# Optimization experiments

Hardware: AMD Instinct MI355X
Metric: run time of the kernel (lower is better)

## Reference

```python
import jax, jax.numpy as jnp
import numpy as np

FRAME, PROJ, MID, HID, T, B = 2048, 512, 128, 1024, 48, 512


def _uniform(key, shape, stdv):
    return jax.random.uniform(key, shape, jnp.float32, -stdv, stdv)


def setup_inputs() -> dict:
    key = jax.random.key(0)
    ks = jax.random.split(key, 16)
    sp = 1.0 / np.sqrt(FRAME)   # frame_embed init
    s1 = 1.0 / np.sqrt(HID)     # LSTMCell init (1/sqrt(hidden))
    sbd = 1.0 / np.sqrt(PROJ)   # BoundaryDetector init (1/sqrt(i_features))
    return {
        "video_feats": jax.random.normal(ks[0], (B, T, FRAME), jnp.float32),
        # frame_embed: Linear(frame_size, projected_size)
        "We": _uniform(ks[1], (PROJ, FRAME), sp),
        "be": _uniform(ks[2], (PROJ,), sp),
        # lstm1: LSTMCell(projected, hidden) with bias
        "W1_ih": _uniform(ks[3], (4 * HID, PROJ), s1),
        "W1_hh": _uniform(ks[4], (4 * HID, HID), s1),
        "b1_ih": _uniform(ks[5], (4 * HID,), s1),
        "b1_hh": _uniform(ks[6], (4 * HID,), s1),
        # lstm2: LSTMCell(hidden, hidden), bias=False
        "W2_ih": _uniform(ks[7], (4 * HID, HID), s1),
        "W2_hh": _uniform(ks[8], (4 * HID, HID), s1),
        # BoundaryDetector params
        "Wsi": _uniform(ks[9], (MID, PROJ), sbd),
        "Wsh": _uniform(ks[10], (MID, HID), sbd),
        "bbd": _uniform(ks[11], (MID,), sbd),
        "vs": _uniform(ks[12], (1, MID), sbd),
    }


def _lstm_cell(x, h, c, W_ih, W_hh, b):
    gates = x @ W_ih.T + h @ W_hh.T + b  # [B, 4H]
    i, f, g, o = jnp.split(gates, 4, axis=-1)  # PyTorch gate order i,f,g,o
    i, f, o = jax.nn.sigmoid(i), jax.nn.sigmoid(f), jax.nn.sigmoid(o)
    g = jnp.tanh(g)
    c_new = f * c + i * g
    h_new = o * jnp.tanh(c_new)
    return h_new, c_new


def _binary_gate(z):
    # eval mode: threshold 0.5; straight-through identity backward
    hard = (z > 0.5).astype(z.dtype)
    return z + jax.lax.stop_gradient(hard - z)


def reference(video_feats, We, be, W1_ih, W1_hh, b1_ih, b1_hh, W2_ih, W2_hh, Wsi, Wsh, bbd, vs):
    bsz = video_feats.shape[0]
    # frame embedding (dropout is identity in eval mode)
    v = video_feats @ We.T + be  # [B, T, PROJ]
    v_t = jnp.swapaxes(v, 0, 1)  # [T, B, PROJ]
    b1 = b1_ih + b1_hh
    zeros = jnp.zeros((bsz, HID), video_feats.dtype)

    def step(carry, vt):
        h1, c1, h2, c2 = carry
        z = jax.nn.sigmoid((vt @ Wsi.T + h1 @ Wsh.T + bbd) @ vs.T)  # [B, 1]
        s = _binary_gate(z)
        h1n, c1n = _lstm_cell(vt, h1, c1, W1_ih, W1_hh, b1)
        h2n, c2n = _lstm_cell(h1n * s, h2, c2, W2_ih, W2_hh, 0.0)
        h1n = h1n * (1.0 - s)
        c1n = c1n * (1.0 - s)
        return (h1n, c1n, h2n, c2n), None

    (h1, _, _, _), _ = jax.lax.scan(step, (zeros, zeros, zeros, zeros), v_t)
    return h1
```

## Files before the change

### kernel.cpp

```cpp
#include <hip/hip_runtime.h>

#define B_     512
#define T_     48
#define FRAME_ 2048
#define PROJ_  512
#define MID_   128
#define HID_   1024
#define G4_    4096

typedef unsigned short u16;
typedef __bf16 bf16x8 __attribute__((ext_vector_type(8)));
typedef float  f32x4  __attribute__((ext_vector_type(4)));

__device__ __forceinline__ float sigmoidf_(float x) {
    return 1.0f / (1.0f + expf(-x));
}
__device__ __forceinline__ u16 f2bf_rn(float f) {
    unsigned int u = __float_as_uint(f);
    u += 0x7fffu + ((u >> 16) & 1u);
    return (u16)(u >> 16);
}
__device__ __forceinline__ float bf2f(u16 s) {
    return __uint_as_float(((unsigned int)s) << 16);
}
__device__ __forceinline__ void gld16(const void* g, void* l) {
    __builtin_amdgcn_global_load_lds((const __attribute__((address_space(1))) void*)g,
                                     (__attribute__((address_space(3))) void*)l, 16, 0, 0);
}
__device__ __forceinline__ uint4 pack8(const u16* h) {
    return make_uint4((unsigned)h[0] | ((unsigned)h[1] << 16),
                      (unsigned)h[2] | ((unsigned)h[3] << 16),
                      (unsigned)h[4] | ((unsigned)h[5] << 16),
                      (unsigned)h[6] | ((unsigned)h[7] << 16));
}

__global__ void wvec_kernel(const float* __restrict__ Wsi, const float* __restrict__ Wsh,
                            const float* __restrict__ vs,
                            double* __restrict__ wsi_vd, float* __restrict__ wsh_v)
{
    const int gid = blockIdx.x * 256 + threadIdx.x;
    if (gid < 512) {
        double s = 0.0;
        for (int mi = 0; mi < MID_; ++mi)
            s += (double)vs[mi] * (double)Wsi[(size_t)mi * PROJ_ + gid];
        wsi_vd[gid] = s;
    } else if (gid < 1536) {
        const int k = gid - 512;
        double s = 0.0;
        for (int mi = 0; mi < MID_; ++mi)
            s += (double)vs[mi] * (double)Wsh[(size_t)mi * HID_ + k];
        wsh_v[k] = (float)s;
    }
}

__global__ void cc_kernel(const float* __restrict__ be, const double* __restrict__ wsi_vd,
                          const float* __restrict__ vs, const float* __restrict__ bbd,
                          double* __restrict__ cc)
{
    __shared__ double red[256];
    const int tid = threadIdx.x;
    double s = 0.0;
    for (int p = tid; p < PROJ_; p += 256) s += (double)be[p] * wsi_vd[p];
    red[tid] = s;
    __syncthreads();
    for (int st = 128; st > 0; st >>= 1) {
        if (tid < st) red[tid] += red[tid + st];
        __syncthreads();
    }
    if (tid == 0) {
        double b = 0.0;
        for (int mi = 0; mi < MID_; ++mi) b += (double)vs[mi] * (double)bbd[mi];
        cc[0] = red[0] + b;
    }
}

__global__ void u_kernel(const float* __restrict__ We, const double* __restrict__ wsi_vd,
                         double* __restrict__ u)
{
    const int f = blockIdx.x * 256 + threadIdx.x;
    double s = 0.0;
    for (int p = 0; p < PROJ_; ++p)
        s += wsi_vd[p] * (double)We[(size_t)p * FRAME_ + f];
    u[f] = s;
}

__global__ __launch_bounds__(256)
void vidpack_kernel(const float* __restrict__ video, const double* __restrict__ u,
                    const double* __restrict__ cc,
                    u16* __restrict__ phi, u16* __restrict__ plo,
                    float* __restrict__ Lv)
{
    __shared__ double red[16][17];
    const int tid = threadIdx.x;
    const int r   = tid & 15, kq = tid >> 4;
    const int row = blockIdx.x * 16 + r;
    const float* vr = video + (size_t)row * FRAME_;
    double s = 0.0;
#pragma unroll
    for (int j = 0; j < 16; ++j) {
        const int k0 = kq * 128 + j * 8;
        const float4 a = *(const float4*)&vr[k0];
        const float4 b = *(const float4*)&vr[k0 + 4];
        const float f[8] = {a.x, a.y, a.z, a.w, b.x, b.y, b.z, b.w};
        s += (double)f[0]*u[k0+0] + (double)f[1]*u[k0+1] + (double)f[2]*u[k0+2]
           + (double)f[3]*u[k0+3] + (double)f[4]*u[k0+4] + (double)f[5]*u[k0+5]
           + (double)f[6]*u[k0+6] + (double)f[7]*u[k0+7];
        u16 h[8], l[8];
#pragma unroll
        for (int e = 0; e < 8; ++e) {
            h[e] = f2bf_rn(f[e]);
            l[e] = f2bf_rn(f[e] - bf2f(h[e]));
        }
        const int g = kq * 16 + j;
        const size_t off = ((size_t)g * 24576 + row) * 16;
        *(uint4*)((char*)phi + off) = pack8(h);
        *(uint4*)((char*)plo + off) = pack8(l);
    }
    red[r][kq] = s;
    __syncthreads();
    if (tid < 16) {
        double t = 0.0;
#pragma unroll
        for (int q = 0; q < 16; ++q) t += red[tid][q];
        const int rw = blockIdx.x * 16 + tid;
        Lv[(rw % T_) * B_ + rw / T_] = (float)(t + cc[0]);
    }
}

__global__ void wepack_kernel(const float* __restrict__ We,
                              u16* __restrict__ phi, u16* __restrict__ plo)
{
    const int kk = blockIdx.x, by = blockIdx.y, tid = threadIdx.x;
#pragma unroll
    for (int pass = 0; pass < 2; ++pass) {
        const int g = tid + pass * 256;
        const int ko = g >> 7, n = g & 127;
        const int p = by * 128 + n;
        const int k = kk * 32 + ko * 8;
        const float4 a = *(const float4*)&We[(size_t)p * FRAME_ + k];
        const float4 b = *(const float4*)&We[(size_t)p * FRAME_ + k + 4];
        const float f[8] = {a.x, a.y, a.z, a.w, b.x, b.y, b.z, b.w};
        u16 h[8], l[8];
#pragma unroll
        for (int e = 0; e < 8; ++e) {
            h[e] = f2bf_rn(f[e]);
            l[e] = f2bf_rn(f[e] - bf2f(h[e]));
        }
        const size_t off = (((size_t)by * 64 + kk) * 512 + g) * 16;
        *(uint4*)((char*)phi + off) = pack8(h);
        *(uint4*)((char*)plo + off) = pack8(l);
    }
}

__global__ void wihpack_kernel(const float* __restrict__ Wih,
                               u16* __restrict__ phi, u16* __restrict__ plo)
{
    const int kk = blockIdx.x, by = blockIdx.y, tid = threadIdx.x;
#pragma unroll
    for (int pass = 0; pass < 2; ++pass) {
        const int g = tid + pass * 256;
        const int ko = g >> 7, n = g & 127;
        const int gate = n & 3, hl = n >> 2;
        const int srow = gate * HID_ + by * 32 + hl;
        const int k = kk * 32 + ko * 8;
        const float4 a = *(const float4*)&Wih[(size_t)srow * PROJ_ + k];
        const float4 b = *(const float4*)&Wih[(size_t)srow * PROJ_ + k + 4];
        const float f[8] = {a.x, a.y, a.z, a.w, b.x, b.y, b.z, b.w};
        u16 h[8], l[8];
#pragma unroll
        for (int e = 0; e < 8; ++e) {
            h[e] = f2bf_rn(f[e]);
            l[e] = f2bf_rn(f[e] - bf2f(h[e]));
        }
        const size_t off = (((size_t)by * 16 + kk) * 512 + g) * 16;
        *(uint4*)((char*)phi + off) = pack8(h);
        *(uint4*)((char*)plo + off) = pack8(l);
    }
}

__global__ void whhpack_kernel(const float* __restrict__ Whh,
                               u16* __restrict__ phi, u16* __restrict__ plo)
{
    const int kk = blockIdx.x, by = blockIdx.y, tid = threadIdx.x;
#pragma unroll
    for (int pass = 0; pass < 2; ++pass) {
        const int g = tid + pass * 256;
        const int ko = g >> 7, n = g & 127;
        const int gate = n & 3, hl = n >> 2;
        const int srow = gate * HID_ + by * 32 + hl;
        const int k = kk * 32 + ko * 8;
        const float4 a = *(const float4*)&Whh[(size_t)srow * HID_ + k];
        const float4 b = *(const float4*)&Whh[(size_t)srow * HID_ + k + 4];
        const float f[8] = {a.x, a.y, a.z, a.w, b.x, b.y, b.z, b.w};
        u16 h[8], l[8];
#pragma unroll
        for (int e = 0; e < 8; ++e) {
            h[e] = f2bf_rn(f[e]);
            l[e] = f2bf_rn(f[e] - bf2f(h[e]));
        }
        const size_t off = (((size_t)by * 32 + kk) * 512 + g) * 16;
        *(uint4*)((char*)phi + off) = pack8(h);
        *(uint4*)((char*)plo + off) = pack8(l);
    }
}

__global__ void b1g_kernel(const float* __restrict__ bih, const float* __restrict__ bhh,
                           float* __restrict__ b1g)
{
    const int n = blockIdx.x * 256 + threadIdx.x;
    const int by = n >> 7, nl = n & 127;
    const int gate = nl & 3, hl = nl >> 2;
    const int src = gate * HID_ + by * 32 + hl;
    b1g[n] = bih[src] + bhh[src];
}

__global__ __launch_bounds__(512, 1)
void embed_mfma_kernel(const u16* __restrict__ Ahi_g, const u16* __restrict__ Alo_g,
                       const u16* __restrict__ Bhi_g, const u16* __restrict__ Blo_g,
                       const float* __restrict__ be,
                       u16* __restrict__ vphi, u16* __restrict__ vplo)
{
    __shared__ char smem[73728];
    const int tid = threadIdx.x;
    const int xcd = blockIdx.x & 7, s_ = blockIdx.x >> 3;
    const int by = s_ & 3, bx = xcd * 48 + (s_ >> 2);
    const int n0 = by * 128;
    const int w = tid >> 6, l = tid & 63, lm = l & 15, ko4 = l >> 4;
    const int wr = (w >> 2) * 32, wc = (w & 3) * 32;
    const int t8 = tid & 255;
    const int koA = t8 >> 6, am = t8 & 63;

    const char* aV = (const char*)(tid < 256 ? Ahi_g : Alo_g)
                     + (size_t)koA * 393216 + ((size_t)bx * 64 + am) * 16;
    const char* bh = (const char*)Bhi_g + (size_t)by * 524288 + tid * 16;
    const char* bl = (const char*)Blo_g + (size_t)by * 524288 + tid * 16;

    auto stage = [&](int s, int buf) {
        char* base = smem + buf * 24576;
        gld16(aV + (size_t)s * 1572864, base + (tid >> 8) * 4096 + t8 * 16);
        gld16(bh + (size_t)s * 8192, base + 8192 + tid * 16);
        gld16(bl + (size_t)s * 8192, base + 16384 + tid * 16);
    };

    f32x4 acc[2][2] = {};
    stage(0, 0);
    stage(1, 1);
    for (int kk = 0; kk < 64; ++kk) {
        if (kk < 63) asm volatile("s_waitcnt vmcnt(3)" ::: "memory");
        else         asm volatile("s_waitcnt vmcnt(0)" ::: "memory");
        __builtin_amdgcn_sched_barrier(0);
        __builtin_amdgcn_s_barrier();

        const char* rb = smem + (kk % 3) * 24576;
        bf16x8 fAh[2], fAl[2], fBh[2], fBl[2];
#pragma unroll
        for (int mt = 0; mt < 2; ++mt) {
            const int idx = ko4 * 64 + wr + mt * 16 + lm;
            fAh[mt] = *(const bf16x8*)(rb + idx * 16);
            fAl[mt] = *(const bf16x8*)(rb + 4096 + idx * 16);
        }
#pragma unroll
        for (int nt = 0; nt < 2; ++nt) {
            const int idx = ko4 * 128 + wc + nt * 16 + lm;
            fBh[nt] = *(const bf16x8*)(rb + 8192 + idx * 16);
            fBl[nt] = *(const bf16x8*)(rb + 16384 + idx * 16);
        }
        if (kk + 2 < 64) stage(kk + 2, (kk + 2) % 3);
        asm volatile("s_waitcnt lgkmcnt(0)" ::: "memory");
        __builtin_amdgcn_sched_barrier(0);
        __builtin_amdgcn_s_setprio(1);
#pragma unroll
        for (int mt = 0; mt < 2; ++mt)
#pragma unroll
            for (int nt = 0; nt < 2; ++nt) {
                acc[mt][nt] = __builtin_amdgcn_mfma_f32_16x16x32_bf16(fAh[mt], fBh[nt], acc[mt][nt], 0, 0, 0);
                acc[mt][nt] = __builtin_amdgcn_mfma_f32_16x16x32_bf16(fAh[mt], fBl[nt], acc[mt][nt], 0, 0, 0);
                acc[mt][nt] = __builtin_amdgcn_mfma_f32_16x16x32_bf16(fAl[mt], fBh[nt], acc[mt][nt], 0, 0, 0);
            }
        __builtin_amdgcn_s_setprio(0);
    }

    __syncthreads();
    float* S = (float*)smem;
#pragma unroll
    for (int mt = 0; mt < 2; ++mt)
#pragma unroll
        for (int nt = 0; nt < 2; ++nt) {
            const int col = wc + nt * 16 + lm;
#pragma unroll
            for (int r = 0; r < 4; ++r) {
                const int row = wr + mt * 16 + ko4 * 4 + r;
                S[row * 132 + col] = acc[mt][nt][r];
            }
        }
    __syncthreads();

#pragma unroll
    for (int pass = 0; pass < 2; ++pass) {
        const int pidx = tid + pass * 512;
        const int m = pidx >> 4, gr = pidx & 15;
        const int p0 = n0 + gr * 8;
        const float4 s0 = *(const float4*)&S[m * 132 + gr * 8];
        const float4 s1 = *(const float4*)&S[m * 132 + gr * 8 + 4];
        const float4 e0 = *(const float4*)&be[p0];
        const float4 e1 = *(const float4*)&be[p0 + 4];
        const float o[8] = {s0.x + e0.x, s0.y + e0.y, s0.z + e0.z, s0.w + e0.w,
                            s1.x + e1.x, s1.y + e1.y, s1.z + e1.z, s1.w + e1.w};
        u16 h[8], lo[8];
#pragma unroll
        for (int e = 0; e < 8; ++e) {
            h[e] = f2bf_rn(o[e]);
            lo[e] = f2bf_rn(o[e] - bf2f(h[e]));
        }
        const int R = bx * 64 + m;
        const int t = R % T_, b = R / T_;
        const size_t off = (size_t)t * 524288 + (((size_t)(p0 >> 3)) * 512 + b) * 16;
        *(uint4*)((char*)vphi + off) = pack8(h);
        *(uint4*)((char*)vplo + off) = pack8(lo);
    }
}

__global__ __launch_bounds__(512, 1)
void gx_mfma_kernel(const u16* __restrict__ vphi, const u16* __restrict__ vplo,
                    const u16* __restrict__ Wihhi, const u16* __restrict__ Wihlo,
                    const float* __restrict__ b1g, float* __restrict__ Gx)
{
    __shared__ char smem[73728];
    const int tid = threadIdx.x;
    const int by = blockIdx.x & 31;
    const int tb = blockIdx.x >> 5;
    const int t = tb >> 3, bx = tb & 7;
    const int b0 = bx * 64, n0 = by * 128;
    const int w = tid >> 6, l = tid & 63, lm = l & 15, ko4 = l >> 4;
    const int wr = (w >> 2) * 32, wc = (w & 3) * 32;
    const int t8 = tid & 255;
    const int koA = t8 >> 6, am = t8 & 63;

    const char* aV = (const char*)(tid < 256 ? vphi : vplo)
                     + (size_t)t * 524288 + ((size_t)koA * 512 + b0 + am) * 16;
    const char* bh = (const char*)Wihhi + (size_t)by * 131072 + tid * 16;
    const char* bl = (const char*)Wihlo + (size_t)by * 131072 + tid * 16;

    auto stage = [&](int s, int buf) {
        char* base = smem + buf * 24576;
        gld16(aV + s * 32768, base + (tid >> 8) * 4096 + t8 * 16);
        gld16(bh + s * 8192, base + 8192 + tid * 16);
        gld16(bl + s * 8192, base + 16384 + tid * 16);
    };

    f32x4 acc[2][2] = {};
    stage(0, 0);
    stage(1, 1);
    for (int kk = 0; kk < 16; ++kk) {
        if (kk < 15) asm volatile("s_waitcnt vmcnt(3)" ::: "memory");
        else         asm volatile("s_waitcnt vmcnt(0)" ::: "memory");
        __builtin_amdgcn_sched_barrier(0);
        __builtin_amdgcn_s_barrier();

        const char* rb = smem + (kk % 3) * 24576;
        bf16x8 fAh[2], fAl[2], fBh[2], fBl[2];
#pragma unroll
        for (int mt = 0; mt < 2; ++mt) {
            const int idx = ko4 * 64 + wr + mt * 16 + lm;
            fAh[mt] = *(const bf16x8*)(rb + idx * 16);
            fAl[mt] = *(const bf16x8*)(rb + 4096 + idx * 16);
        }
#pragma unroll
        for (int nt = 0; nt < 2; ++nt) {
            const int idx = ko4 * 128 + wc + nt * 16 + lm;
            fBh[nt] = *(const bf16x8*)(rb + 8192 + idx * 16);
            fBl[nt] = *(const bf16x8*)(rb + 16384 + idx * 16);
        }
        if (kk + 2 < 16) stage(kk + 2, (kk + 2) % 3);
        asm volatile("s_waitcnt lgkmcnt(0)" ::: "memory");
        __builtin_amdgcn_sched_barrier(0);
        __builtin_amdgcn_s_setprio(1);
#pragma unroll
        for (int mt = 0; mt < 2; ++mt)
#pragma unroll
            for (int nt = 0; nt < 2; ++nt) {
                acc[mt][nt] = __builtin_amdgcn_mfma_f32_16x16x32_bf16(fAh[mt], fBh[nt], acc[mt][nt], 0, 0, 0);
                acc[mt][nt] = __builtin_amdgcn_mfma_f32_16x16x32_bf16(fAh[mt], fBl[nt], acc[mt][nt], 0, 0, 0);
                acc[mt][nt] = __builtin_amdgcn_mfma_f32_16x16x32_bf16(fAl[mt], fBh[nt], acc[mt][nt], 0, 0, 0);
            }
        __builtin_amdgcn_s_setprio(0);
    }

    __syncthreads();
    float* S = (float*)smem;
#pragma unroll
    for (int mt = 0; mt < 2; ++mt)
#pragma unroll
        for (int nt = 0; nt < 2; ++nt) {
            const int col = wc + nt * 16 + lm;
#pragma unroll
            for (int r = 0; r < 4; ++r) {
                const int row = wr + mt * 16 + ko4 * 4 + r;
                S[row * 132 + col] = acc[mt][nt][r];
            }
        }
    __syncthreads();

#pragma unroll
    for (int pass = 0; pass < 2; ++pass) {
        const int pidx = tid + pass * 512;
        const int m = pidx >> 4, gr = pidx & 15;
        const int c0 = gr * 8;
        const float4 s0 = *(const float4*)&S[m * 132 + c0];
        const float4 s1 = *(const float4*)&S[m * 132 + c0 + 4];
        const float4 a0 = *(const float4*)&b1g[n0 + c0];
        const float4 a1 = *(const float4*)&b1g[n0 + c0 + 4];
        float* dst = Gx + ((size_t)t * 512 + b0 + m) * 4096 + n0 + c0;
        *(float4*)dst       = make_float4(s0.x + a0.x, s0.y + a0.y, s0.z + a0.z, s0.w + a0.w);
        *(float4*)(dst + 4) = make_float4(s1.x + a1.x, s1.y + a1.y, s1.z + a1.z, s1.w + a1.w);
    }
}

__global__ __launch_bounds__(512, 1)
void lstm_mfma_kernel(const u16* __restrict__ hhi,  const u16* __restrict__ hlo,
                      const u16* __restrict__ Whhhi, const u16* __restrict__ Whhlo,
                      const float* __restrict__ Gxt,
                      const float* __restrict__ Lv_t,
                      const float* __restrict__ Pin,
                      float* __restrict__ Pout,
                      const float* __restrict__ wsh_v,
                      float* __restrict__ c1, float* __restrict__ h1o,
                      u16* __restrict__ hhio, u16* __restrict__ hloo)
{
    __shared__ char smem[73984];
    float* keepsm = (float*)(smem + 73728);
    const int tid = threadIdx.x;
    const int bid = blockIdx.x;
    const int xcd = bid & 7, slot = bid >> 3;
    const int by  = xcd * 4 + (slot & 3);
    const int bx  = slot >> 2;
    const int b0  = bx * 64;
    const int w = tid >> 6, l = tid & 63, lm = l & 15, ko4 = l >> 4;
    const int wr = (w >> 2) * 32, wc = (w & 3) * 32;
    const int t8 = tid & 255;
    const int koA = t8 >> 6, am = t8 & 63;

    const char* aH = (const char*)(tid < 256 ? hhi : hlo)
                     + ((size_t)koA * 512 + b0 + am) * 16;
    const char* bh = (const char*)Whhhi + (size_t)by * 262144 + tid * 16;
    const char* bl = (const char*)Whhlo + (size_t)by * 262144 + tid * 16;

    auto stage = [&](int s, int buf) {
        char* base = smem + buf * 24576;
        gld16(aH + s * 32768, base + (tid >> 8) * 4096 + t8 * 16);
        gld16(bh + s * 8192, base + 8192 + tid * 16);
        gld16(bl + s * 8192, base + 16384 + tid * 16);
    };

    f32x4 acc[2][2] = {};
    stage(0, 0);
    stage(1, 1);

    if (tid < 64) {
        double s = (double)Lv_t[b0 + tid];
#pragma unroll
        for (int j = 0; j < 32; ++j) s += (double)Pin[j * B_ + b0 + tid];
        keepsm[tid] = (s > 0.0) ? 0.0f : 1.0f;
    }

    for (int kk = 0; kk < 32; ++kk) {
        if (kk < 31) asm volatile("s_waitcnt vmcnt(3)" ::: "memory");
        else         asm volatile("s_waitcnt vmcnt(0)" ::: "memory");
        __builtin_amdgcn_sched_barrier(0);
        __builtin_amdgcn_s_barrier();

        const char* rb = smem + (kk % 3) * 24576;
        bf16x8 fAh[2], fAl[2], fBh[2], fBl[2];
#pragma unroll
        for (int mt = 0; mt < 2; ++mt) {
            const int idx = ko4 * 64 + wr + mt * 16 + lm;
            fAh[mt] = *(const bf16x8*)(rb + idx * 16);
            fAl[mt] = *(const bf16x8*)(rb + 4096 + idx * 16);
        }
#pragma unroll
        for (int nt = 0; nt < 2; ++nt) {
            const int idx = ko4 * 128 + wc + nt * 16 + lm;
            fBh[nt] = *(const bf16x8*)(rb + 8192 + idx * 16);
            fBl[nt] = *(const bf16x8*)(rb + 16384 + idx * 16);
        }
        if (kk + 2 < 32) stage(kk + 2, (kk + 2) % 3);
        asm volatile("s_waitcnt lgkmcnt(0)" ::: "memory");
        __builtin_amdgcn_sched_barrier(0);
        __builtin_amdgcn_s_setprio(1);
#pragma unroll
        for (int mt = 0; mt < 2; ++mt)
#pragma unroll
            for (int nt = 0; nt < 2; ++nt) {
                acc[mt][nt] = __builtin_amdgcn_mfma_f32_16x16x32_bf16(fAh[mt], fBh[nt], acc[mt][nt], 0, 0, 0);
                acc[mt][nt] = __builtin_amdgcn_mfma_f32_16x16x32_bf16(fAh[mt], fBl[nt], acc[mt][nt], 0, 0, 0);
                acc[mt][nt] = __builtin_amdgcn_mfma_f32_16x16x32_bf16(fAl[mt], fBh[nt], acc[mt][nt], 0, 0, 0);
            }
        __builtin_amdgcn_s_setprio(0);
    }

    const int h_l = tid & 31, rg = tid >> 5;
    const int hg  = by * 32 + h_l;
    float4 gx[4];
#pragma unroll
    for (int i = 0; i < 4; ++i)
        gx[i] = *(const float4*)&Gxt[((size_t)b0 + rg * 4 + i) * 4096 + by * 128 + h_l * 4];

    __syncthreads();
    float* S = (float*)smem;
#pragma unroll
    for (int mt = 0; mt < 2; ++mt)
#pragma unroll
        for (int nt = 0; nt < 2; ++nt) {
            const int col = wc + nt * 16 + lm;
#pragma unroll
            for (int r = 0; r < 4; ++r) {
                const int row = wr + mt * 16 + ko4 * 4 + r;
                S[row * 132 + col] = acc[mt][nt][r];
            }
        }
    __syncthreads();

    const float wv = wsh_v[hg];
    const size_t hgbase = (((size_t)by * 4 + (h_l >> 3)) * 512) * 16 + (h_l & 7) * 2;
#pragma unroll
    for (int i = 0; i < 4; ++i) {
        const int m = rg * 4 + i;
        const int b = b0 + m;
        const float4 g4 = *(const float4*)&S[m * 132 + h_l * 4];
        const float i_ = sigmoidf_(g4.x + gx[i].x);
        const float f_ = sigmoidf_(g4.y + gx[i].y);
        const float g_ = tanhf(g4.z + gx[i].z);
        const float o_ = sigmoidf_(g4.w + gx[i].w);
        const size_t off = (size_t)b * HID_ + hg;
        float cn = f_ * c1[off] + i_ * g_;
        float hn = o_ * tanhf(cn);
        const float kp = keepsm[m];
        cn *= kp; hn *= kp;
        c1[off] = cn;
        if (h1o) h1o[off] = hn;
        const u16 hb = f2bf_rn(hn);
        const size_t hoff = hgbase + (size_t)b * 16;
        *(u16*)((char*)hhio + hoff) = hb;
        *(u16*)((char*)hloo + hoff) = f2bf_rn(hn - bf2f(hb));
        float pr = hn * wv;
        pr += __shfl_xor(pr, 16);
        pr += __shfl_xor(pr, 8);
        pr += __shfl_xor(pr, 4);
        pr += __shfl_xor(pr, 2);
        pr += __shfl_xor(pr, 1);
        if (h_l == 0) Pout[by * B_ + b] = pr;
    }
}

extern "C" void kernel_launch(void* const* d_in, const int* in_sizes, int n_in,
                              void* d_out, int out_size, void* d_ws, size_t ws_size,
                              hipStream_t stream)
{
    const float* video = (const float*)d_in[0];
    const float* We    = (const float*)d_in[1];
    const float* be    = (const float*)d_in[2];
    const float* W1_ih = (const float*)d_in[3];
    const float* W1_hh = (const float*)d_in[4];
    const float* b1_ih = (const float*)d_in[5];
    const float* b1_hh = (const float*)d_in[6];
    const float* Wsi   = (const float*)d_in[9];
    const float* Wsh   = (const float*)d_in[10];
    const float* bbd   = (const float*)d_in[11];
    const float* vs    = (const float*)d_in[12];
    float* out = (float*)d_out;

    char* p = (char*)d_ws;
    auto alloc = [&](size_t bytes) { char* r = p; p += (bytes + 255) & ~(size_t)255; return r; };
    u16* vidhi = (u16*)alloc((size_t)24576 * FRAME_ * 2);
    u16* vidlo = (u16*)alloc((size_t)24576 * FRAME_ * 2);
    u16* vphi  = (u16*)alloc((size_t)T_ * B_ * PROJ_ * 2);
    u16* vplo  = (u16*)alloc((size_t)T_ * B_ * PROJ_ * 2);
    u16* Wehi  = (u16*)alloc((size_t)PROJ_ * FRAME_ * 2);
    u16* Welo  = (u16*)alloc((size_t)PROJ_ * FRAME_ * 2);
    u16* Wihhi = (u16*)alloc((size_t)G4_ * PROJ_ * 2);
    u16* Wihlo = (u16*)alloc((size_t)G4_ * PROJ_ * 2);
    u16* Whhhi = (u16*)alloc((size_t)G4_ * HID_ * 2);
    u16* Whhlo = (u16*)alloc((size_t)G4_ * HID_ * 2);
    float* Gx  = (float*)alloc((size_t)T_ * B_ * G4_ * 4);
    float* c1  = (float*)alloc((size_t)B_ * HID_ * 4);
    u16* hhiA  = (u16*)alloc((size_t)B_ * HID_ * 2);
    u16* hhiB  = (u16*)alloc((size_t)B_ * HID_ * 2);
    u16* hloA  = (u16*)alloc((size_t)B_ * HID_ * 2);
    u16* hloB  = (u16*)alloc((size_t)B_ * HID_ * 2);
    double* wsi_vd = (double*)alloc(512 * 8);
    double* ud     = (double*)alloc(2048 * 8);
    double* ccd    = (double*)alloc(256);
    float* wsh_v = (float*)alloc(1024 * 4);
    float* Lv    = (float*)alloc((size_t)T_ * B_ * 4);
    float* PA    = (float*)alloc(32 * B_ * 4);
    float* PB    = (float*)alloc(32 * B_ * 4);
    float* b1g   = (float*)alloc(G4_ * 4);

    hipMemsetAsync(c1,   0, (size_t)B_ * HID_ * 4, stream);
    hipMemsetAsync(hhiA, 0, (size_t)B_ * HID_ * 2, stream);
    hipMemsetAsync(hloA, 0, (size_t)B_ * HID_ * 2, stream);
    hipMemsetAsync(PA,   0, 32 * B_ * 4, stream);

    b1g_kernel<<<16, 256, 0, stream>>>(b1_ih, b1_hh, b1g);
    wvec_kernel<<<6, 256, 0, stream>>>(Wsi, Wsh, vs, wsi_vd, wsh_v);
    cc_kernel<<<1, 256, 0, stream>>>(be, wsi_vd, vs, bbd, ccd);
    u_kernel<<<8, 256, 0, stream>>>(We, wsi_vd, ud);
    wepack_kernel<<<dim3(64, 4), 256, 0, stream>>>(We, Wehi, Welo);
    wihpack_kernel<<<dim3(16, 32), 256, 0, stream>>>(W1_ih, Wihhi, Wihlo);
    whhpack_kernel<<<dim3(32, 32), 256, 0, stream>>>(W1_hh, Whhhi, Whhlo);
    vidpack_kernel<<<1536, 256, 0, stream>>>(video, ud, ccd, vidhi, vidlo, Lv);
    embed_mfma_kernel<<<1536, 512, 0, stream>>>(vidhi, vidlo, Wehi, Welo, be, vphi, vplo);
    gx_mfma_kernel<<<12288, 512, 0, stream>>>(vphi, vplo, Wihhi, Wihlo, b1g, Gx);

    u16* hhi_in = hhiA; u16* hhi_out = hhiB;
    u16* hlo_in = hloA; u16* hlo_out = hloB;
    float* Pin = PA; float* Pout = PB;

    for (int t = 0; t < T_; ++t) {
        float* ho = (t == T_ - 1) ? out : nullptr;
        lstm_mfma_kernel<<<256, 512, 0, stream>>>(hhi_in, hlo_in, Whhhi, Whhlo,
                                                  Gx + (size_t)t * B_ * G4_,
                                                  Lv + t * B_, Pin, Pout, wsh_v,
                                                  c1, ho, hhi_out, hlo_out);
        { u16* tmp = hhi_in; hhi_in = hhi_out; hhi_out = tmp; }
        { u16* tmp = hlo_in; hlo_in = hlo_out; hlo_out = tmp; }
        { float* tmp = Pin; Pin = Pout; Pout = tmp; }
    }
}
```

Measured before the change: 1.664 ms.

## Load weight fragments directly into registers and shrink LDS for higher occupancy

In the embed, gx and LSTM GEMM kernels, the B (weight) fragments are now read straight from global memory into registers and prefetched one k-step ahead. Only the A tile still goes through LDS, as a 4-slot ring with a single barrier per step. This cuts shared memory from 72KB to about 33KB and raises the launch-bounds occupancy hints to 4 or 2 blocks per CU, aiming to hide latency with more resident waves and fewer LDS round-trips. The trade-offs are uncoalesced direct global loads, more register pressure that could cause spills under the new bounds, and hand-written vmcnt counts that must match the number of in-flight loads.

New measurement: 1.782 ms. +7.1%, slower.

```diff
diff --git a/kernel.cpp b/kernel.cpp
--- a/kernel.cpp
+++ b/kernel.cpp
@@ -214,13 +214,14 @@
     b1g[n] = bih[src] + bhh[src];
 }
 
-__global__ __launch_bounds__(512, 1)
+
+__global__ __launch_bounds__(512, 4)
 void embed_mfma_kernel(const u16* __restrict__ Ahi_g, const u16* __restrict__ Alo_g,
                        const u16* __restrict__ Bhi_g, const u16* __restrict__ Blo_g,
                        const float* __restrict__ be,
                        u16* __restrict__ vphi, u16* __restrict__ vplo)
 {
-    __shared__ char smem[73728];
+    __shared__ char smem[33792];
     const int tid = threadIdx.x;
     const int xcd = blockIdx.x & 7, s_ = blockIdx.x >> 3;
     const int by = s_ & 3, bx = xcd * 48 + (s_ >> 2);
@@ -232,53 +233,55 @@
 
     const char* aV = (const char*)(tid < 256 ? Ahi_g : Alo_g)
                      + (size_t)koA * 393216 + ((size_t)bx * 64 + am) * 16;
-    const char* bh = (const char*)Bhi_g + (size_t)by * 524288 + tid * 16;
-    const char* bl = (const char*)Blo_g + (size_t)by * 524288 + tid * 16;
-
-    auto stage = [&](int s, int buf) {
-        char* base = smem + buf * 24576;
-        gld16(aV + (size_t)s * 1572864, base + (tid >> 8) * 4096 + t8 * 16);
-        gld16(bh + (size_t)s * 8192, base + 8192 + tid * 16);
-        gld16(bl + (size_t)s * 8192, base + 16384 + tid * 16);
-    };
+    const char* bh = (const char*)Bhi_g + (size_t)by * 524288
+                     + ((size_t)(ko4 * 128 + wc + lm)) * 16;
+    const char* bl = (const char*)Blo_g + (size_t)by * 524288
+                     + ((size_t)(ko4 * 128 + wc + lm)) * 16;
+    char* lbase = smem + (tid >> 8) * 4096 + t8 * 16;
 
     f32x4 acc[2][2] = {};
-    stage(0, 0);
-    stage(1, 1);
+    bf16x8 nBh[2], nBl[2], cBh[2], cBl[2], fAh[2], fAl[2];
+
+    gld16(aV, lbase);
+    gld16(aV + 1572864, lbase + 8192);
+#pragma unroll
+    for (int nt = 0; nt < 2; ++nt) {
+        nBh[nt] = *(const bf16x8*)(bh + nt * 256);
+        nBl[nt] = *(const bf16x8*)(bl + nt * 256);
+    }
+
+#pragma unroll
     for (int kk = 0; kk < 64; ++kk) {
-        if (kk < 63) asm volatile("s_waitcnt vmcnt(3)" ::: "memory");
-        else         asm volatile("s_waitcnt vmcnt(0)" ::: "memory");
+        if (kk == 63) asm volatile("s_waitcnt vmcnt(4)\ns_barrier" ::: "memory");
+        else          asm volatile("s_waitcnt vmcnt(5)\ns_barrier" ::: "memory");
         __builtin_amdgcn_sched_barrier(0);
-        __builtin_amdgcn_s_barrier();
-
-        const char* rb = smem + (kk % 3) * 24576;
-        bf16x8 fAh[2], fAl[2], fBh[2], fBl[2];
+#pragma unroll
+        for (int nt = 0; nt < 2; ++nt) { cBh[nt] = nBh[nt]; cBl[nt] = nBl[nt]; }
+        const char* rb = smem + (kk & 3) * 8192;
 #pragma unroll
         for (int mt = 0; mt < 2; ++mt) {
-            const int idx = ko4 * 64 + wr + mt * 16 + lm;
-            fAh[mt] = *(const bf16x8*)(rb + idx * 16);
-            fAl[mt] = *(const bf16x8*)(rb + 4096 + idx * 16);
-        }
-#pragma unroll
-        for (int nt = 0; nt < 2; ++nt) {
-            const int idx = ko4 * 128 + wc + nt * 16 + lm;
-            fBh[nt] = *(const bf16x8*)(rb + 8192 + idx * 16);
-            fBl[nt] = *(const bf16x8*)(rb + 16384 + idx * 16);
-        }
-        if (kk + 2 < 64) stage(kk + 2, (kk + 2) % 3);
-        asm volatile("s_waitcnt lgkmcnt(0)" ::: "memory");
-        __builtin_amdgcn_sched_barrier(0);
-        __builtin_amdgcn_s_setprio(1);
+            fAh[mt] = *(const bf16x8*)(rb + (ko4 * 64 + wr + mt * 16 + lm) * 16);
+            fAl[mt] = *(const bf16x8*)(rb + 4096 + (ko4 * 64 + wr + mt * 16 + lm) * 16);
+        }
+        if (kk + 1 < 64) {
+#pragma unroll
+            for (int nt = 0; nt < 2; ++nt) {
+                nBh[nt] = *(const bf16x8*)(bh + (size_t)(kk + 1) * 8192 + nt * 256);
+                nBl[nt] = *(const bf16x8*)(bl + (size_t)(kk + 1) * 8192 + nt * 256);
+            }
+        }
+        if (kk + 2 < 64) gld16(aV + (size_t)(kk + 2) * 1572864, lbase + ((kk + 2) & 3) * 8192);
 #pragma unroll
         for (int mt = 0; mt < 2; ++mt)
 #pragma unroll
             for (int nt = 0; nt < 2; ++nt) {
-                acc[mt][nt] = __builtin_amdgcn_mfma_f32_16x16x32_bf16(fAh[mt], fBh[nt], acc[mt][nt], 0, 0, 0);
-                acc[mt][nt] = __builtin_amdgcn_mfma_f32_16x16x32_bf16(fAh[mt], fBl[nt], acc[mt][nt], 0, 0, 0);
-                acc[mt][nt] = __builtin_amdgcn_mfma_f32_16x16x32_bf16(fAl[mt], fBh[nt], acc[mt][nt], 0, 0, 0);
-            }
-        __builtin_amdgcn_s_setprio(0);
-    }
+                acc[mt][nt] = __builtin_amdgcn_mfma_f32_16x16x32_bf16(fAh[mt], cBh[nt], acc[mt][nt], 0, 0, 0);
+                acc[mt][nt] = __builtin_amdgcn_mfma_f32_16x16x32_bf16(fAh[mt], cBl[nt], acc[mt][nt], 0, 0, 0);
+                acc[mt][nt] = __builtin_amdgcn_mfma_f32_16x16x32_bf16(fAl[mt], cBh[nt], acc[mt][nt], 0, 0, 0);
+            }
+    }
+    asm volatile("s_waitcnt lgkmcnt(0)" ::: "memory");
+    __builtin_amdgcn_sched_barrier(0);
 
     __syncthreads();
     float* S = (float*)smem;
@@ -320,71 +323,73 @@
     }
 }
 
-__global__ __launch_bounds__(512, 1)
+__global__ __launch_bounds__(512, 4)
 void gx_mfma_kernel(const u16* __restrict__ vphi, const u16* __restrict__ vplo,
                     const u16* __restrict__ Wihhi, const u16* __restrict__ Wihlo,
                     const float* __restrict__ b1g, float* __restrict__ Gx)
 {
-    __shared__ char smem[73728];
+    __shared__ char smem[33792];
     const int tid = threadIdx.x;
-    const int by = blockIdx.x & 31;
-    const int tb = blockIdx.x >> 5;
-    const int t = tb >> 3, bx = tb & 7;
-    const int b0 = bx * 64, n0 = by * 128;
+    const int by32 = blockIdx.x & 31;
+    const int tb2  = blockIdx.x >> 5;
+    const int t2 = tb2 >> 3, bx2 = tb2 & 7;
+    const int b02 = bx2 * 64, n02 = by32 * 128;
     const int w = tid >> 6, l = tid & 63, lm = l & 15, ko4 = l >> 4;
     const int wr = (w >> 2) * 32, wc = (w & 3) * 32;
     const int t8 = tid & 255;
     const int koA = t8 >> 6, am = t8 & 63;
 
     const char* aV = (const char*)(tid < 256 ? vphi : vplo)
-                     + (size_t)t * 524288 + ((size_t)koA * 512 + b0 + am) * 16;
-    const char* bh = (const char*)Wihhi + (size_t)by * 131072 + tid * 16;
-    const char* bl = (const char*)Wihlo + (size_t)by * 131072 + tid * 16;
-
-    auto stage = [&](int s, int buf) {
-        char* base = smem + buf * 24576;
-        gld16(aV + s * 32768, base + (tid >> 8) * 4096 + t8 * 16);
-        gld16(bh + s * 8192, base + 8192 + tid * 16);
-        gld16(bl + s * 8192, base + 16384 + tid * 16);
-    };
+                     + (size_t)t2 * 524288 + ((size_t)koA * 512 + b02 + am) * 16;
+    const char* bh = (const char*)Wihhi + (size_t)by32 * 131072
+                     + ((size_t)(ko4 * 128 + wc + lm)) * 16;
+    const char* bl = (const char*)Wihlo + (size_t)by32 * 131072
+                     + ((size_t)(ko4 * 128 + wc + lm)) * 16;
+    char* lbase = smem + (tid >> 8) * 4096 + t8 * 16;
 
     f32x4 acc[2][2] = {};
-    stage(0, 0);
-    stage(1, 1);
+    bf16x8 nBh[2], nBl[2], cBh[2], cBl[2], fAh[2], fAl[2];
+
+    gld16(aV, lbase);
+    gld16(aV + 32768, lbase + 8192);
+#pragma unroll
+    for (int nt = 0; nt < 2; ++nt) {
+        nBh[nt] = *(const bf16x8*)(bh + nt * 256);
+        nBl[nt] = *(const bf16x8*)(bl + nt * 256);
+    }
+
+#pragma unroll
     for (int kk = 0; kk < 16; ++kk) {
-        if (kk < 15) asm volatile("s_waitcnt vmcnt(3)" ::: "memory");
-        else         asm volatile("s_waitcnt vmcnt(0)" ::: "memory");
+        if (kk == 15) asm volatile("s_waitcnt vmcnt(4)\ns_barrier" ::: "memory");
+        else          asm volatile("s_waitcnt vmcnt(5)\ns_barrier" ::: "memory");
         __builtin_amdgcn_sched_barrier(0);
-        __builtin_amdgcn_s_barrier();
-
-        const char* rb = smem + (kk % 3) * 24576;
-        bf16x8 fAh[2], fAl[2], fBh[2], fBl[2];
+#pragma unroll
+        for (int nt = 0; nt < 2; ++nt) { cBh[nt] = nBh[nt]; cBl[nt] = nBl[nt]; }
+        const char* rb = smem + (kk & 3) * 8192;
 #pragma unroll
         for (int mt = 0; mt < 2; ++mt) {
-            const int idx = ko4 * 64 + wr + mt * 16 + lm;
-            fAh[mt] = *(const bf16x8*)(rb + idx * 16);
-            fAl[mt] = *(const bf16x8*)(rb + 4096 + idx * 16);
-        }
-#pragma unroll
-        for (int nt = 0; nt < 2; ++nt) {
-            const int idx = ko4 * 128 + wc + nt * 16 + lm;
-            fBh[nt] = *(const bf16x8*)(rb + 8192 + idx * 16);
-            fBl[nt] = *(const bf16x8*)(rb + 16384 + idx * 16);
-        }
-        if (kk + 2 < 16) stage(kk + 2, (kk + 2) % 3);
-        asm volatile("s_waitcnt lgkmcnt(0)" ::: "memory");
-        __builtin_amdgcn_sched_barrier(0);
-        __builtin_amdgcn_s_setprio(1);
+            fAh[mt] = *(const bf16x8*)(rb + (ko4 * 64 + wr + mt * 16 + lm) * 16);
+            fAl[mt] = *(const bf16x8*)(rb + 4096 + (ko4 * 64 + wr + mt * 16 + lm) * 16);
+        }
+        if (kk + 1 < 16) {
+#pragma unroll
+            for (int nt = 0; nt < 2; ++nt) {
+                nBh[nt] = *(const bf16x8*)(bh + (size_t)(kk + 1) * 8192 + nt * 256);
+                nBl[nt] = *(const bf16x8*)(bl + (size_t)(kk + 1) * 8192 + nt * 256);
+            }
+        }
+        if (kk + 2 < 16) gld16(aV + (size_t)(kk + 2) * 32768, lbase + ((kk + 2) & 3) * 8192);
 #pragma unroll
         for (int mt = 0; mt < 2; ++mt)
 #pragma unroll
             for (int nt = 0; nt < 2; ++nt) {
-                acc[mt][nt] = __builtin_amdgcn_mfma_f32_16x16x32_bf16(fAh[mt], fBh[nt], acc[mt][nt], 0, 0, 0);
-                acc[mt][nt] = __builtin_amdgcn_mfma_f32_16x16x32_bf16(fAh[mt], fBl[nt], acc[mt][nt], 0, 0, 0);
-                acc[mt][nt] = __builtin_amdgcn_mfma_f32_16x16x32_bf16(fAl[mt], fBh[nt], acc[mt][nt], 0, 0, 0);
-            }
-        __builtin_amdgcn_s_setprio(0);
-    }
+                acc[mt][nt] = __builtin_amdgcn_mfma_f32_16x16x32_bf16(fAh[mt], cBh[nt], acc[mt][nt], 0, 0, 0);
+                acc[mt][nt] = __builtin_amdgcn_mfma_f32_16x16x32_bf16(fAh[mt], cBl[nt], acc[mt][nt], 0, 0, 0);
+                acc[mt][nt] = __builtin_amdgcn_mfma_f32_16x16x32_bf16(fAl[mt], cBh[nt], acc[mt][nt], 0, 0, 0);
+            }
+    }
+    asm volatile("s_waitcnt lgkmcnt(0)" ::: "memory");
+    __builtin_amdgcn_sched_barrier(0);
 
     __syncthreads();
     float* S = (float*)smem;
@@ -408,15 +413,15 @@
         const int c0 = gr * 8;
         const float4 s0 = *(const float4*)&S[m * 132 + c0];
         const float4 s1 = *(const float4*)&S[m * 132 + c0 + 4];
-        const float4 a0 = *(const float4*)&b1g[n0 + c0];
-        const float4 a1 = *(const float4*)&b1g[n0 + c0 + 4];
-        float* dst = Gx + ((size_t)t * 512 + b0 + m) * 4096 + n0 + c0;
+        const float4 a0 = *(const float4*)&b1g[n02 + c0];
+        const float4 a1 = *(const float4*)&b1g[n02 + c0 + 4];
+        float* dst = Gx + ((size_t)t2 * 512 + b02 + m) * 4096 + n02 + c0;
         *(float4*)dst       = make_float4(s0.x + a0.x, s0.y + a0.y, s0.z + a0.z, s0.w + a0.w);
         *(float4*)(dst + 4) = make_float4(s1.x + a1.x, s1.y + a1.y, s1.z + a1.z, s1.w + a1.w);
     }
 }
 
-__global__ __launch_bounds__(512, 1)
+__global__ __launch_bounds__(512, 2)
 void lstm_mfma_kernel(const u16* __restrict__ hhi,  const u16* __restrict__ hlo,
                       const u16* __restrict__ Whhhi, const u16* __restrict__ Whhlo,
                       const float* __restrict__ Gxt,
@@ -427,8 +432,8 @@
                       float* __restrict__ c1, float* __restrict__ h1o,
                       u16* __restrict__ hhio, u16* __restrict__ hloo)
 {
-    __shared__ char smem[73984];
-    float* keepsm = (float*)(smem + 73728);
+    __shared__ char smem[34048];
+    float* keepsm = (float*)(smem + 33792);
     const int tid = threadIdx.x;
     const int bid = blockIdx.x;
     const int xcd = bid & 7, slot = bid >> 3;
@@ -440,63 +445,64 @@
     const int t8 = tid & 255;
     const int koA = t8 >> 6, am = t8 & 63;
 
+    if (tid < 64) {
+        double s = (double)Lv_t[b0 + tid];
+#pragma unroll
+        for (int j = 0; j < 32; ++j) s += (double)Pin[j * B_ + b0 + tid];
+        keepsm[tid] = (s > 0.0) ? 0.0f : 1.0f;
+    }
+
     const char* aH = (const char*)(tid < 256 ? hhi : hlo)
                      + ((size_t)koA * 512 + b0 + am) * 16;
-    const char* bh = (const char*)Whhhi + (size_t)by * 262144 + tid * 16;
-    const char* bl = (const char*)Whhlo + (size_t)by * 262144 + tid * 16;
-
-    auto stage = [&](int s, int buf) {
-        char* base = smem + buf * 24576;
-        gld16(aH + s * 32768, base + (tid >> 8) * 4096 + t8 * 16);
-        gld16(bh + s * 8192, base + 8192 + tid * 16);
-        gld16(bl + s * 8192, base + 16384 + tid * 16);
-    };
+    const char* bh = (const char*)Whhhi + (size_t)by * 262144
+                     + ((size_t)(ko4 * 128 + wc + lm)) * 16;
+    const char* bl = (const char*)Whhlo + (size_t)by * 262144
+                     + ((size_t)(ko4 * 128 + wc + lm)) * 16;
+    char* lbase = smem + (tid >> 8) * 4096 + t8 * 16;
 
     f32x4 acc[2][2] = {};
-    stage(0, 0);
-    stage(1, 1);
-
-    if (tid < 64) {
-        double s = (double)Lv_t[b0 + tid];
-#pragma unroll
-        for (int j = 0; j < 32; ++j) s += (double)Pin[j * B_ + b0 + tid];
-        keepsm[tid] = (s > 0.0) ? 0.0f : 1.0f;
-    }
-
+    bf16x8 nBh[2], nBl[2], cBh[2], cBl[2], fAh[2], fAl[2];
+
+    gld16(aH, lbase);
+    gld16(aH + 32768, lbase + 8192);
+#pragma unroll
+    for (int nt = 0; nt < 2; ++nt) {
+        nBh[nt] = *(const bf16x8*)(bh + nt * 256);
+        nBl[nt] = *(const bf16x8*)(bl + nt * 256);
+    }
+
+#pragma unroll
     for (int kk = 0; kk < 32; ++kk) {
-        if (kk < 31) asm volatile("s_waitcnt vmcnt(3)" ::: "memory");
-        else         asm volatile("s_waitcnt vmcnt(0)" ::: "memory");
+        if (kk == 31) asm volatile("s_waitcnt vmcnt(4)\ns_barrier" ::: "memory");
+        else          asm volatile("s_waitcnt vmcnt(5)\ns_barrier" ::: "memory");
         __builtin_amdgcn_sched_barrier(0);
-        __builtin_amdgcn_s_barrier();
-
-        const char* rb = smem + (kk % 3) * 24576;
-        bf16x8 fAh[2], fAl[2], fBh[2], fBl[2];
+#pragma unroll
+        for (int nt = 0; nt < 2; ++nt) { cBh[nt] = nBh[nt]; cBl[nt] = nBl[nt]; }
+        const char* rb = smem + (kk & 3) * 8192;
 #pragma unroll
         for (int mt = 0; mt < 2; ++mt) {
-            const int idx = ko4 * 64 + wr + mt * 16 + lm;
-            fAh[mt] = *(const bf16x8*)(rb + idx * 16);
-            fAl[mt] = *(const bf16x8*)(rb + 4096 + idx * 16);
-        }
-#pragma unroll
-        for (int nt = 0; nt < 2; ++nt) {
-            const int idx = ko4 * 128 + wc + nt * 16 + lm;
-            fBh[nt] = *(const bf16x8*)(rb + 8192 + idx * 16);
-            fBl[nt] = *(const bf16x8*)(rb + 16384 + idx * 16);
-        }
-        if (kk + 2 < 32) stage(kk + 2, (kk + 2) % 3);
-        asm volatile("s_waitcnt lgkmcnt(0)" ::: "memory");
-        __builtin_amdgcn_sched_barrier(0);
-        __builtin_amdgcn_s_setprio(1);
+            fAh[mt] = *(const bf16x8*)(rb + (ko4 * 64 + wr + mt * 16 + lm) * 16);
+            fAl[mt] = *(const bf16x8*)(rb + 4096 + (ko4 * 64 + wr + mt * 16 + lm) * 16);
+        }
+        if (kk + 1 < 32) {
+#pragma unroll
+            for (int nt = 0; nt < 2; ++nt) {
+                nBh[nt] = *(const bf16x8*)(bh + (size_t)(kk + 1) * 8192 + nt * 256);
+                nBl[nt] = *(const bf16x8*)(bl + (size_t)(kk + 1) * 8192 + nt * 256);
+            }
+        }
+        if (kk + 2 < 32) gld16(aH + (size_t)(kk + 2) * 32768, lbase + ((kk + 2) & 3) * 8192);
 #pragma unroll
         for (int mt = 0; mt < 2; ++mt)
 #pragma unroll
             for (int nt = 0; nt < 2; ++nt) {
-                acc[mt][nt] = __builtin_amdgcn_mfma_f32_16x16x32_bf16(fAh[mt], fBh[nt], acc[mt][nt], 0, 0, 0);
-                acc[mt][nt] = __builtin_amdgcn_mfma_f32_16x16x32_bf16(fAh[mt], fBl[nt], acc[mt][nt], 0, 0, 0);
-                acc[mt][nt] = __builtin_amdgcn_mfma_f32_16x16x32_bf16(fAl[mt], fBh[nt], acc[mt][nt], 0, 0, 0);
-            }
-        __builtin_amdgcn_s_setprio(0);
-    }
+                acc[mt][nt] = __builtin_amdgcn_mfma_f32_16x16x32_bf16(fAh[mt], cBh[nt], acc[mt][nt], 0, 0, 0);
+                acc[mt][nt] = __builtin_amdgcn_mfma_f32_16x16x32_bf16(fAh[mt], cBl[nt], acc[mt][nt], 0, 0, 0);
+                acc[mt][nt] = __builtin_amdgcn_mfma_f32_16x16x32_bf16(fAl[mt], cBh[nt], acc[mt][nt], 0, 0, 0);
+            }
+    }
+    asm volatile("s_waitcnt lgkmcnt(0)" ::: "memory");
+    __builtin_amdgcn_sched_barrier(0);
 
     const int h_l = tid & 31, rg = tid >> 5;
     const int hg  = by * 32 + h_l;
```
